# Kernel tuning notes

Measured on AMD Instinct MI355X. Metric: run time of the kernel, lower is better.

The kernel has to match this reference:

```python
import jax, jax.numpy as jnp
import numpy as np

N_NODES = 100000
N_EDGES = 1600000
D_IN, D_HID, D_OUT = 64, 64, 4


def _nnconv(x, src, dst, e, W_edge, b_edge, W_root, bias, n_nodes, d_in, d_out):
    """PyG NNConv with edge net Linear(1, d_in*d_out), aggr='add'.

    Theta_e = reshape(e * W_edge + b_edge, [d_in, d_out])  (linear in scalar e)
    => message_e = x[src] @ Theta_e = e * (x[src] @ Wm) + x[src] @ Bm
    out_i = sum_{e: dst=i} message_e + x_i @ W_root + bias
    """
    Wm = W_edge.reshape(d_in, d_out)   # edge-linear weight, factored
    Bm = b_edge.reshape(d_in, d_out)   # edge-linear bias, factored
    xj = x[src]                        # [E, d_in] irregular gather
    msg = e * (xj @ Wm) + xj @ Bm      # [E, d_out]; e is [E,1], broadcasts
    agg = jax.ops.segment_sum(msg, dst, num_segments=n_nodes)  # scatter-add
    return agg + x @ W_root + bias


def setup_inputs() -> dict:
    key = jax.random.key(0)
    ks = jax.random.split(key, 16)
    s = 0.05
    inp = {
        "x": jax.random.normal(ks[0], (N_NODES, D_IN), jnp.float32),
        "edge_index": jax.random.randint(ks[1], (2, N_EDGES), 0, N_NODES, jnp.int64 if jax.config.jax_enable_x64 else jnp.int32),
        "edge_attr": jax.random.uniform(ks[2], (N_EDGES, 1), jnp.float32),
        # layer 1: D_IN -> D_HID
        "We1": jax.random.normal(ks[3], (D_IN * D_HID,), jnp.float32) * s,
        "be1": jax.random.normal(ks[4], (D_IN * D_HID,), jnp.float32) * s,
        "Wr1": jax.random.normal(ks[5], (D_IN, D_HID), jnp.float32) * s,
        "b1": jnp.zeros((D_HID,), jnp.float32),
        # layer 2: D_HID -> D_HID
        "We2": jax.random.normal(ks[6], (D_HID * D_HID,), jnp.float32) * s,
        "be2": jax.random.normal(ks[7], (D_HID * D_HID,), jnp.float32) * s,
        "Wr2": jax.random.normal(ks[8], (D_HID, D_HID), jnp.float32) * s,
        "b2": jnp.zeros((D_HID,), jnp.float32),
        # layer 3: D_HID -> D_OUT
        "We3": jax.random.normal(ks[9], (D_HID * D_OUT,), jnp.float32) * s,
        "be3": jax.random.normal(ks[10], (D_HID * D_OUT,), jnp.float32) * s,
        "Wr3": jax.random.normal(ks[11], (D_HID, D_OUT), jnp.float32) * s,
        "b3": jnp.zeros((D_OUT,), jnp.float32),
    }
    return inp


def reference(x, edge_index, edge_attr,
              We1, be1, Wr1, b1,
              We2, be2, Wr2, b2,
              We3, be3, Wr3, b3):
    src, dst = edge_index[0], edge_index[1]  # source_to_target flow
    n = x.shape[0]
    h = _nnconv(x, src, dst, edge_attr, We1, be1, Wr1, b1, n, D_IN, D_HID)
    h = jax.nn.relu(h)  # dropout is a no-op at inference
    h = _nnconv(h, src, dst, edge_attr, We2, be2, Wr2, b2, n, D_HID, D_HID)
    h = jax.nn.relu(h)
    h = _nnconv(h, src, dst, edge_attr, We3, be3, Wr3, b3, n, D_HID, D_OUT)
    return jax.nn.log_softmax(h, axis=1)
```

## Files before the change

kernel.cpp:

```cpp
#include <hip/hip_runtime.h>
#include <math.h>

#define D 64
#define NBUCK 392
#define CAPB 4736
#define PART_BLOCKS 256

typedef __attribute__((ext_vector_type(4))) float f32x4;
typedef __attribute__((ext_vector_type(8))) _Float16 f16x8;
typedef __attribute__((ext_vector_type(2))) _Float16 f16x2;

__device__ __forceinline__ unsigned short f2h(float f) {
  return __builtin_bit_cast(unsigned short, (_Float16)f);
}
__device__ __forceinline__ f16x2 as_h2(unsigned u) { return __builtin_bit_cast(f16x2, u); }
__device__ __forceinline__ unsigned bcu(f16x2 v) { return __builtin_bit_cast(unsigned, v); }
__device__ __forceinline__ unsigned packH2(float a, float b) {
  f16x2 v; v.x = (_Float16)a; v.y = (_Float16)b;
  return __builtin_bit_cast(unsigned, v);
}


__global__ void wprep(const float* __restrict__ We1, const float* __restrict__ be1,
                      const float* __restrict__ Wr1, const float* __restrict__ We2,
                      const float* __restrict__ be2, const float* __restrict__ Wr2,
                      const float* __restrict__ We3, const float* __restrict__ be3,
                      const float* __restrict__ Wr3, unsigned short* __restrict__ Wt) {
  int l = blockIdx.x;
  if (l == 2) {
    unsigned short* Wt3 = Wt + 24576;
    for (int idx = threadIdx.x; idx < 1024; idx += 256) {
      int r = idx >> 6, k = idx & 63;
      int sel = r >> 2, o = r & 3;
      float v = (sel == 0) ? We3[k * 4 + o]
              : (sel == 1) ? be3[k * 4 + o]
              : (sel == 2) ? Wr3[k * 4 + o] : 0.f;
      Wt3[idx] = f2h(v);
    }
    return;
  }
  const float* We = l ? We2 : We1;
  const float* be = l ? be2 : be1;
  const float* Wr = l ? Wr2 : Wr1;
  for (int idx = threadIdx.x; idx < 12288; idx += 256) {
    int o = idx / 192, k = idx % 192;
    float v = (k < 64)  ? We[k * 64 + o]
            : (k < 128) ? be[(k - 64) * 64 + o]
                        : Wr[(k - 128) * 64 + o];
    Wt[l * 12288 + idx] = f2h(v);
  }
}

__global__ __launch_bounds__(256) void xprep(const float* __restrict__ x,
                                             unsigned short* __restrict__ xb, int n64) {
  int idx = (blockIdx.x * 256 + threadIdx.x) * 4;
  if (idx >= n64) return;
  float4 v = *(const float4*)(x + idx);
  ushort4 o;
  o.x = f2h(v.x); o.y = f2h(v.y); o.z = f2h(v.z); o.w = f2h(v.w);
  *(ushort4*)(xb + idx) = o;
}

__global__ __launch_bounds__(256) void transformC(
    const unsigned short* __restrict__ Sb, const unsigned short* __restrict__ hb,
    const unsigned short* __restrict__ WtP, const float* __restrict__ b,
    unsigned short* __restrict__ hbOut, int n) {
  __shared__ uint4 ldsW4[1536];
  char* ldsW = (char*)ldsW4;
  int t = threadIdx.x;
  const uint4* wg = (const uint4*)WtP;
#pragma unroll
  for (int i = 0; i < 6; ++i) {
    int idx = t + i * 256;
    int off = idx * 16;
    int row = idx / 24;
    *(uint4*)(ldsW + (off ^ ((row & 7) << 4))) = wg[idx];
  }
  __syncthreads();
  int wid = t >> 6, lane = t & 63;
  int n0 = blockIdx.x * 64 + wid * 16;
  if (n0 >= n) return;
  int arow = lane & 15, g = lane >> 4;
  int nodeA = min(n0 + arow, n - 1);
  const unsigned short* Sp = Sb + (size_t)nodeA * 128;
  f16x8 a[6];
#pragma unroll
  for (int c = 0; c < 4; ++c)
    a[c] = *(const f16x8*)(Sp + c * 32 + g * 8);
  const unsigned short* hp = hb + (size_t)nodeA * 64;
  a[4] = *(const f16x8*)(hp + g * 8);
  a[5] = *(const f16x8*)(hp + 32 + g * 8);

  f32x4 acc[4];
#pragma unroll
  for (int tt = 0; tt < 4; ++tt) acc[tt] = (f32x4){0.f, 0.f, 0.f, 0.f};
#pragma unroll
  for (int tt = 0; tt < 4; ++tt) {
    int o = tt * 16 + arow;
    int sw = (o & 7) << 4;
    int rb = o * 384;
#pragma unroll
    for (int c = 0; c < 6; ++c) {
      f16x8 bf = *(const f16x8*)(ldsW + ((rb + c * 64 + g * 16) ^ sw));
      acc[tt] = __builtin_amdgcn_mfma_f32_16x16x32_f16(a[c], bf, acc[tt], 0, 0, 0);
    }
  }
#pragma unroll
  for (int tt = 0; tt < 4; ++tt) {
    float bb = b[tt * 16 + arow];
#pragma unroll
    for (int r2 = 0; r2 < 4; ++r2) {
      int nd = n0 + g * 4 + r2;
      if (nd < n)
        hbOut[(size_t)nd * 64 + tt * 16 + arow] = f2h(fmaxf(acc[tt][r2] + bb, 0.f));
    }
  }
}

__global__ __launch_bounds__(256) void transform3M(
    const unsigned short* __restrict__ hb, const unsigned short* __restrict__ Wt3,
    const float* __restrict__ b, unsigned* __restrict__ yz3p,
    float* __restrict__ agg3, int n) {
  int t = threadIdx.x;
  int wid = t >> 6, lane = t & 63;
  int n0 = blockIdx.x * 64 + wid * 16;
  if (n0 >= n) return;
  int arow = lane & 15, g = lane >> 4;
  int nodeA = min(n0 + arow, n - 1);
  const unsigned short* hp = hb + (size_t)nodeA * 64;
  f16x8 a0 = *(const f16x8*)(hp + g * 8);
  f16x8 a1 = *(const f16x8*)(hp + 32 + g * 8);
  f16x8 b0 = *(const f16x8*)(Wt3 + arow * 64 + g * 8);
  f16x8 b1 = *(const f16x8*)(Wt3 + arow * 64 + 32 + g * 8);
  f32x4 acc = (f32x4){0.f, 0.f, 0.f, 0.f};
  acc = __builtin_amdgcn_mfma_f32_16x16x32_f16(a0, b0, acc, 0, 0, 0);
  acc = __builtin_amdgcn_mfma_f32_16x16x32_f16(a1, b1, acc, 0, 0, 0);
  float bb = (arow < 4) ? b[arow] : 0.f;
#pragma unroll
  for (int r2 = 0; r2 < 4; ++r2) {
    float zv = __shfl_xor(acc[r2], 4, 64);
    float rv = __shfl_xor(acc[r2], 8, 64);
    int nd = n0 + g * 4 + r2;
    if (arow < 4 && nd < n) {
      yz3p[(size_t)nd * 4 + arow] = packH2(acc[r2], zv);
      agg3[(size_t)nd * 4 + arow] = rv + bb;
    }
  }
}


__global__ __launch_bounds__(256) void histA(const int* __restrict__ ei,
                                             int* __restrict__ hist, int ne) {
  __shared__ int h[NBUCK];
  int t = threadIdx.x;
  for (int i = t; i < NBUCK; i += 256) h[i] = 0;
  __syncthreads();
  int chunk = (ne + PART_BLOCKS - 1) / PART_BLOCKS;
  int e0 = blockIdx.x * chunk;
  int e1 = min(ne, e0 + chunk);
  for (int e = e0 + t; e < e1; e += 256)
    atomicAdd(&h[ei[ne + e] >> 8], 1);
  __syncthreads();
  for (int i = t; i < NBUCK; i += 256) hist[blockIdx.x * NBUCK + i] = h[i];
}

__global__ __launch_bounds__(256) void scanCols(int* __restrict__ hist,
                                                int* __restrict__ gTotal) {
  __shared__ int wsum[4];
  int b = blockIdx.x;
  int t = threadIdx.x;
  int v = hist[t * NBUCK + b];
  int lane = t & 63, wid = t >> 6;
  int inc = v;
#pragma unroll
  for (int d = 1; d < 64; d <<= 1) {
    int u = __shfl_up(inc, d, 64);
    if (lane >= d) inc += u;
  }
  if (lane == 63) wsum[wid] = inc;
  __syncthreads();
  if (t == 0) {
    int a = 0;
#pragma unroll
    for (int w = 0; w < 4; ++w) { int tmp = wsum[w]; wsum[w] = a; a += tmp; }
  }
  __syncthreads();
  int excl = wsum[wid] + inc - v;
  hist[t * NBUCK + b] = b * CAPB + excl;
  if (t == 255) gTotal[b] = excl + v;
}

__global__ __launch_bounds__(256) void scatterC(
    const int* __restrict__ ei, const float* __restrict__ ea,
    const int* __restrict__ baseArr, uint2* __restrict__ edgesP, int ne) {
  __shared__ int cnt[NBUCK];
  __shared__ int lbase[NBUCK];
  int t = threadIdx.x;
  for (int i = t; i < NBUCK; i += 256) {
    cnt[i] = 0;
    lbase[i] = baseArr[blockIdx.x * NBUCK + i];
  }
  __syncthreads();
  int chunk = (ne + PART_BLOCKS - 1) / PART_BLOCKS;
  int e0 = blockIdx.x * chunk;
  int e1 = min(ne, e0 + chunk);
  for (int e = e0 + t; e < e1; e += 256) {
    unsigned s = (unsigned)ei[e];
    int dd = ei[ne + e];
    float ev = ea[e];
    unsigned abits = packH2(ev, ev);
    int bk = dd >> 8;
    int pos = atomicAdd(&cnt[bk], 1);
    edgesP[lbase[bk] + pos] = make_uint2(s | ((unsigned)(dd & 255) << 20), abits);
  }
}

__global__ __launch_bounds__(256) void placeK(
    const uint2* __restrict__ edgesP, const int* __restrict__ gTotal,
    uint2* __restrict__ edgeS, int* __restrict__ offS, int* __restrict__ offE,
    int n) {
  __shared__ int deg[256];
  __shared__ int cur[256];
  __shared__ int wsum[4];
  int b = blockIdx.x;
  int t = threadIdx.x;
  int base = b * CAPB;
  int cnt = gTotal[b];
  int n0 = b << 8;
  int nn = min(256, n - n0);
  deg[t] = 0;
  __syncthreads();
  for (int i = t; i < cnt; i += 256)
    atomicAdd(&deg[edgesP[base + i].x >> 20], 1);
  __syncthreads();
  int v = deg[t];
  int lane = t & 63, wid = t >> 6;
  int inc = v;
#pragma unroll
  for (int d2 = 1; d2 < 64; d2 <<= 1) {
    int u = __shfl_up(inc, d2, 64);
    if (lane >= d2) inc += u;
  }
  if (lane == 63) wsum[wid] = inc;
  __syncthreads();
  if (t == 0) {
    int a = 0;
#pragma unroll
    for (int w = 0; w < 4; ++w) { int tmp = wsum[w]; wsum[w] = a; a += tmp; }
  }
  __syncthreads();
  int excl = wsum[wid] + inc - v;
  cur[t] = excl;
  if (t < nn) {
    offS[n0 + t] = base + excl;
    offE[n0 + t] = base + excl + v;
  }
  __syncthreads();
  for (int i = t; i < cnt; i += 256) {
    uint2 ent = edgesP[base + i];
    int dl = ent.x >> 20;
    int slot = base + atomicAdd(&cur[dl], 1);
    edgeS[slot] = make_uint2(ent.x & 0xFFFFFu, ent.y);
  }
}

__global__ __launch_bounds__(256) void gather2(
    const int* __restrict__ offS, const int* __restrict__ offE,
    const uint2* __restrict__ edgeS, const unsigned short* __restrict__ hb,
    unsigned short* __restrict__ Sb, int n) {
  int node = (blockIdx.x * 256 + threadIdx.x) >> 6;
  int lane = threadIdx.x & 63;
  if (node >= n) return;
  int grp = lane >> 3, l8 = lane & 7;
  int j0 = offS[node];
  int jend = offE[node];
  f16x2 s1[4], s0[4];
#pragma unroll
  for (int q = 0; q < 4; ++q) { s1[q] = (f16x2)0; s0[q] = (f16x2)0; }
  int j = j0 + grp;
#pragma unroll 1
  for (; j + 8 < jend; j += 16) {
    uint2 edA = edgeS[j];
    uint2 edB = edgeS[j + 8];
    uint4 rA = *(const uint4*)(hb + (size_t)edA.x * 64 + l8 * 8);
    uint4 rB = *(const uint4*)(hb + (size_t)edB.x * 64 + l8 * 8);
    f16x2 eA = as_h2(edA.y);
    f16x2 eB = as_h2(edB.y);
    f16x2 hA[4] = {as_h2(rA.x), as_h2(rA.y), as_h2(rA.z), as_h2(rA.w)};
    f16x2 hB[4] = {as_h2(rB.x), as_h2(rB.y), as_h2(rB.z), as_h2(rB.w)};
#pragma unroll
    for (int q = 0; q < 4; ++q) {
      s1[q] += hA[q] * eA; s0[q] += hA[q];
      s1[q] += hB[q] * eB; s0[q] += hB[q];
    }
  }
  if (j < jend) {
    uint2 ed = edgeS[j];
    uint4 r = *(const uint4*)(hb + (size_t)ed.x * 64 + l8 * 8);
    f16x2 e = as_h2(ed.y);
    f16x2 h[4] = {as_h2(r.x), as_h2(r.y), as_h2(r.z), as_h2(r.w)};
#pragma unroll
    for (int q = 0; q < 4; ++q) { s1[q] += h[q] * e; s0[q] += h[q]; }
  }
#pragma unroll
  for (int q = 0; q < 4; ++q) {
    s1[q] += as_h2(__shfl_xor(bcu(s1[q]), 8, 64));
    s1[q] += as_h2(__shfl_xor(bcu(s1[q]), 16, 64));
    s1[q] += as_h2(__shfl_xor(bcu(s1[q]), 32, 64));
    s0[q] += as_h2(__shfl_xor(bcu(s0[q]), 8, 64));
    s0[q] += as_h2(__shfl_xor(bcu(s0[q]), 16, 64));
    s0[q] += as_h2(__shfl_xor(bcu(s0[q]), 32, 64));
  }
  if (grp == 0) {
    unsigned short* sp = Sb + (size_t)node * 128 + l8 * 8;
    *(uint4*)sp = make_uint4(bcu(s1[0]), bcu(s1[1]), bcu(s1[2]), bcu(s1[3]));
    *(uint4*)(sp + 64) = make_uint4(bcu(s0[0]), bcu(s0[1]), bcu(s0[2]), bcu(s0[3]));
  }
}

__global__ __launch_bounds__(256) void gather4_logsm(
    const int* __restrict__ offS, const int* __restrict__ offE,
    const uint2* __restrict__ edgeS, const unsigned* __restrict__ yz3p,
    const float* __restrict__ agg3, float* __restrict__ out, int n) {
  int idx = blockIdx.x * 256 + threadIdx.x;
  int node = idx >> 2;
  int o = idx & 3;
  if (node >= n) return;
  int j = offS[node];
  int jend = offE[node];
  float acc = agg3[(size_t)node * 4 + o];
#pragma unroll 1
  for (; j < jend; ++j) {
    uint2 ed = edgeS[j];
    f16x2 yz = as_h2(yz3p[(size_t)ed.x * 4 + o]);
    float e = (float)as_h2(ed.y).x;
    acc += fmaf(e, (float)yz.x, (float)yz.y);
  }
  float m = acc;
  m = fmaxf(m, __shfl_xor(m, 1, 4));
  m = fmaxf(m, __shfl_xor(m, 2, 4));
  float s = expf(acc - m);
  s += __shfl_xor(s, 1, 4);
  s += __shfl_xor(s, 2, 4);
  out[(size_t)node * 4 + o] = acc - m - logf(s);
}


extern "C" void kernel_launch(void* const* d_in, const int* in_sizes, int n_in,
                              void* d_out, int out_size, void* d_ws, size_t ws_size,
                              hipStream_t stream) {
  const float* x = (const float*)d_in[0];
  const int* ei = (const int*)d_in[1];
  const float* ea = (const float*)d_in[2];
  const float* We1 = (const float*)d_in[3];
  const float* be1 = (const float*)d_in[4];
  const float* Wr1 = (const float*)d_in[5];
  const float* b1 = (const float*)d_in[6];
  const float* We2 = (const float*)d_in[7];
  const float* be2 = (const float*)d_in[8];
  const float* Wr2 = (const float*)d_in[9];
  const float* b2 = (const float*)d_in[10];
  const float* We3 = (const float*)d_in[11];
  const float* be3 = (const float*)d_in[12];
  const float* Wr3 = (const float*)d_in[13];
  const float* b3 = (const float*)d_in[14];

  const int N = in_sizes[0] / D;
  const int E = in_sizes[2];
  const size_t EREG = (size_t)NBUCK * CAPB;

  char* ws = (char*)d_ws;
  uint2* edgeS = (uint2*)ws;
  unsigned short* Sb = (unsigned short*)(ws + EREG * 8);
  unsigned short* xb = Sb + (size_t)N * 128;
  unsigned short* hb2 = xb + (size_t)N * 64;
  unsigned* yz3p = (unsigned*)(hb2 + (size_t)N * 64);
  float* agg3 = (float*)(yz3p + (size_t)N * 4);
  int* offS = (int*)(agg3 + (size_t)N * 4);
  int* offE = offS + N;
  int* gTotal = offE + N;
  int* hist = gTotal + NBUCK;
  unsigned short* Wt = (unsigned short*)(hist + PART_BLOCKS * NBUCK);
  uint2* edgesP = (uint2*)Sb;
  unsigned short* hb3 = xb;
  float* out = (float*)d_out;

  int tblocksM = (N + 63) / 64;
  int g64blocks = (int)(((long long)N * 64 + 255) / 256);
  int g4blocks = (int)(((long long)N * 4 + 255) / 256);
  int xblocks = (int)(((long long)N * 64 / 4 + 255) / 256);

  wprep<<<3, 256, 0, stream>>>(We1, be1, Wr1, We2, be2, Wr2, We3, be3, Wr3, Wt);
  xprep<<<xblocks, 256, 0, stream>>>(x, xb, N * 64);
  histA<<<PART_BLOCKS, 256, 0, stream>>>(ei, hist, E);
  scanCols<<<NBUCK, 256, 0, stream>>>(hist, gTotal);
  scatterC<<<PART_BLOCKS, 256, 0, stream>>>(ei, ea, hist, edgesP, E);
  placeK<<<NBUCK, 256, 0, stream>>>(edgesP, gTotal, edgeS, offS, offE, N);

  gather2<<<g64blocks, 256, 0, stream>>>(offS, offE, edgeS, xb, Sb, N);
  transformC<<<tblocksM, 256, 0, stream>>>(Sb, xb, Wt, b1, hb2, N);
  gather2<<<g64blocks, 256, 0, stream>>>(offS, offE, edgeS, hb2, Sb, N);
  transformC<<<tblocksM, 256, 0, stream>>>(Sb, hb2, Wt + 12288, b2, hb3, N);
  transform3M<<<tblocksM, 256, 0, stream>>>(hb3, Wt + 24576, b3, yz3p, agg3, N);
  gather4_logsm<<<g4blocks, 256, 0, stream>>>(offS, offE, edgeS, yz3p, agg3, out, N);
}
```

Measured before the change: 296.4 us.

## Fuse prep kernels, fuse layer-3 transform into layer-2 epilogue, unroll final gather

```diff
diff --git a/kernel.cpp b/kernel.cpp
--- a/kernel.cpp
+++ b/kernel.cpp
@@ -20,52 +20,72 @@
   return __builtin_bit_cast(unsigned, v);
 }
 
-
-__global__ void wprep(const float* __restrict__ We1, const float* __restrict__ be1,
-                      const float* __restrict__ Wr1, const float* __restrict__ We2,
-                      const float* __restrict__ be2, const float* __restrict__ Wr2,
-                      const float* __restrict__ We3, const float* __restrict__ be3,
-                      const float* __restrict__ Wr3, unsigned short* __restrict__ Wt) {
-  int l = blockIdx.x;
-  if (l == 2) {
-    unsigned short* Wt3 = Wt + 24576;
-    for (int idx = threadIdx.x; idx < 1024; idx += 256) {
-      int r = idx >> 6, k = idx & 63;
-      int sel = r >> 2, o = r & 3;
-      float v = (sel == 0) ? We3[k * 4 + o]
-              : (sel == 1) ? be3[k * 4 + o]
-              : (sel == 2) ? Wr3[k * 4 + o] : 0.f;
-      Wt3[idx] = f2h(v);
-    }
-    return;
-  }
-  const float* We = l ? We2 : We1;
-  const float* be = l ? be2 : be1;
-  const float* Wr = l ? Wr2 : Wr1;
-  for (int idx = threadIdx.x; idx < 12288; idx += 256) {
-    int o = idx / 192, k = idx % 192;
-    float v = (k < 64)  ? We[k * 64 + o]
-            : (k < 128) ? be[(k - 64) * 64 + o]
-                        : Wr[(k - 128) * 64 + o];
-    Wt[l * 12288 + idx] = f2h(v);
-  }
-}
-
-__global__ __launch_bounds__(256) void xprep(const float* __restrict__ x,
-                                             unsigned short* __restrict__ xb, int n64) {
-  int idx = (blockIdx.x * 256 + threadIdx.x) * 4;
-  if (idx >= n64) return;
-  float4 v = *(const float4*)(x + idx);
-  ushort4 o;
-  o.x = f2h(v.x); o.y = f2h(v.y); o.z = f2h(v.z); o.w = f2h(v.w);
-  *(ushort4*)(xb + idx) = o;
-}
-
+__global__ __launch_bounds__(256) void prepK(
+    const int* __restrict__ ei, int ne,
+    const float* __restrict__ x, unsigned short* __restrict__ xb, int n64,
+    const float* __restrict__ We1, const float* __restrict__ be1,
+    const float* __restrict__ Wr1, const float* __restrict__ We2,
+    const float* __restrict__ be2, const float* __restrict__ Wr2,
+    const float* __restrict__ We3, const float* __restrict__ be3,
+    const float* __restrict__ Wr3, unsigned short* __restrict__ Wt,
+    int* __restrict__ hist) {
+  __shared__ int h[NBUCK];
+  int bid = blockIdx.x;
+  int t = threadIdx.x;
+  if (bid < PART_BLOCKS) {
+    for (int i = t; i < NBUCK; i += 256) h[i] = 0;
+    __syncthreads();
+    int chunk = (ne + PART_BLOCKS - 1) / PART_BLOCKS;
+    int e0 = bid * chunk;
+    int e1 = min(ne, e0 + chunk);
+    for (int e = e0 + t; e < e1; e += 256)
+      atomicAdd(&h[ei[ne + e] >> 8], 1);
+    __syncthreads();
+    for (int i = t; i < NBUCK; i += 256) hist[bid * NBUCK + i] = h[i];
+  } else if (bid < PART_BLOCKS + 3) {
+    int l = bid - PART_BLOCKS;
+    if (l == 2) {
+      unsigned short* Wt3 = Wt + 24576;
+      for (int idx = t; idx < 1024; idx += 256) {
+        int r = idx >> 6, k = idx & 63;
+        int sel = r >> 2, o = r & 3;
+        float v = (sel == 0) ? We3[k * 4 + o]
+                : (sel == 1) ? be3[k * 4 + o]
+                : (sel == 2) ? Wr3[k * 4 + o] : 0.f;
+        Wt3[idx] = f2h(v);
+      }
+    } else {
+      const float* We = l ? We2 : We1;
+      const float* be = l ? be2 : be1;
+      const float* Wr = l ? Wr2 : Wr1;
+      for (int idx = t; idx < 12288; idx += 256) {
+        int o = idx / 192, k = idx % 192;
+        float v = (k < 64)  ? We[k * 64 + o]
+                : (k < 128) ? be[(k - 64) * 64 + o]
+                            : Wr[(k - 128) * 64 + o];
+        Wt[l * 12288 + idx] = f2h(v);
+      }
+    }
+  } else {
+    int idx = ((bid - PART_BLOCKS - 3) * 256 + t) * 4;
+    if (idx < n64) {
+      float4 v = *(const float4*)(x + idx);
+      ushort4 o;
+      o.x = f2h(v.x); o.y = f2h(v.y); o.z = f2h(v.z); o.w = f2h(v.w);
+      *(ushort4*)(xb + idx) = o;
+    }
+  }
+}
+
+template <bool RELU, bool LAST>
 __global__ __launch_bounds__(256) void transformC(
     const unsigned short* __restrict__ Sb, const unsigned short* __restrict__ hb,
     const unsigned short* __restrict__ WtP, const float* __restrict__ b,
-    unsigned short* __restrict__ hbOut, int n) {
+    unsigned short* __restrict__ hbOut,
+    const unsigned short* __restrict__ Wt3, const float* __restrict__ b3,
+    unsigned* __restrict__ yz3p, float* __restrict__ agg3, int n) {
   __shared__ uint4 ldsW4[1536];
+  __shared__ unsigned short ldsH[4][1024];
   char* ldsW = (char*)ldsW4;
   int t = threadIdx.x;
   const uint4* wg = (const uint4*)WtP;
@@ -105,64 +125,52 @@
       acc[tt] = __builtin_amdgcn_mfma_f32_16x16x32_f16(a[c], bf, acc[tt], 0, 0, 0);
     }
   }
-#pragma unroll
-  for (int tt = 0; tt < 4; ++tt) {
-    float bb = b[tt * 16 + arow];
+  if (!LAST) {
+#pragma unroll
+    for (int tt = 0; tt < 4; ++tt) {
+      float bb = b[tt * 16 + arow];
+#pragma unroll
+      for (int r2 = 0; r2 < 4; ++r2) {
+        int nd = n0 + g * 4 + r2;
+        if (nd < n)
+          hbOut[(size_t)nd * 64 + tt * 16 + arow] = f2h(fmaxf(acc[tt][r2] + bb, 0.f));
+      }
+    }
+  } else {
+    char* ldsC = (char*)ldsH[wid];
+#pragma unroll
+    for (int tt = 0; tt < 4; ++tt) {
+      float bb = b[tt * 16 + arow];
+#pragma unroll
+      for (int r2 = 0; r2 < 4; ++r2) {
+        int ndl = g * 4 + r2;
+        int boff = ndl * 128 + (tt * 16 + arow) * 2;
+        *(unsigned short*)(ldsC + (boff ^ ((ndl & 7) << 4))) =
+            f2h(fmaxf(acc[tt][r2] + bb, 0.f));
+      }
+    }
+    int sw2 = (arow & 7) << 4;
+    f16x8 a3a = *(const f16x8*)(ldsC + ((arow * 128 + g * 16) ^ sw2));
+    f16x8 a3b = *(const f16x8*)(ldsC + ((arow * 128 + 64 + g * 16) ^ sw2));
+    f16x8 b3a = *(const f16x8*)(Wt3 + arow * 64 + g * 8);
+    f16x8 b3b = *(const f16x8*)(Wt3 + arow * 64 + 32 + g * 8);
+    f32x4 acc3 = (f32x4){0.f, 0.f, 0.f, 0.f};
+    acc3 = __builtin_amdgcn_mfma_f32_16x16x32_f16(a3a, b3a, acc3, 0, 0, 0);
+    acc3 = __builtin_amdgcn_mfma_f32_16x16x32_f16(a3b, b3b, acc3, 0, 0, 0);
+    float bb3 = (arow < 4) ? b3[arow] : 0.f;
 #pragma unroll
     for (int r2 = 0; r2 < 4; ++r2) {
+      float zv = __shfl_xor(acc3[r2], 4, 64);
+      float rv = __shfl_xor(acc3[r2], 8, 64);
       int nd = n0 + g * 4 + r2;
-      if (nd < n)
-        hbOut[(size_t)nd * 64 + tt * 16 + arow] = f2h(fmaxf(acc[tt][r2] + bb, 0.f));
-    }
-  }
-}
-
-__global__ __launch_bounds__(256) void transform3M(
-    const unsigned short* __restrict__ hb, const unsigned short* __restrict__ Wt3,
-    const float* __restrict__ b, unsigned* __restrict__ yz3p,
-    float* __restrict__ agg3, int n) {
-  int t = threadIdx.x;
-  int wid = t >> 6, lane = t & 63;
-  int n0 = blockIdx.x * 64 + wid * 16;
-  if (n0 >= n) return;
-  int arow = lane & 15, g = lane >> 4;
-  int nodeA = min(n0 + arow, n - 1);
-  const unsigned short* hp = hb + (size_t)nodeA * 64;
-  f16x8 a0 = *(const f16x8*)(hp + g * 8);
-  f16x8 a1 = *(const f16x8*)(hp + 32 + g * 8);
-  f16x8 b0 = *(const f16x8*)(Wt3 + arow * 64 + g * 8);
-  f16x8 b1 = *(const f16x8*)(Wt3 + arow * 64 + 32 + g * 8);
-  f32x4 acc = (f32x4){0.f, 0.f, 0.f, 0.f};
-  acc = __builtin_amdgcn_mfma_f32_16x16x32_f16(a0, b0, acc, 0, 0, 0);
-  acc = __builtin_amdgcn_mfma_f32_16x16x32_f16(a1, b1, acc, 0, 0, 0);
-  float bb = (arow < 4) ? b[arow] : 0.f;
-#pragma unroll
-  for (int r2 = 0; r2 < 4; ++r2) {
-    float zv = __shfl_xor(acc[r2], 4, 64);
-    float rv = __shfl_xor(acc[r2], 8, 64);
-    int nd = n0 + g * 4 + r2;
-    if (arow < 4 && nd < n) {
-      yz3p[(size_t)nd * 4 + arow] = packH2(acc[r2], zv);
-      agg3[(size_t)nd * 4 + arow] = rv + bb;
-    }
-  }
-}
-
-
-__global__ __launch_bounds__(256) void histA(const int* __restrict__ ei,
-                                             int* __restrict__ hist, int ne) {
-  __shared__ int h[NBUCK];
-  int t = threadIdx.x;
-  for (int i = t; i < NBUCK; i += 256) h[i] = 0;
-  __syncthreads();
-  int chunk = (ne + PART_BLOCKS - 1) / PART_BLOCKS;
-  int e0 = blockIdx.x * chunk;
-  int e1 = min(ne, e0 + chunk);
-  for (int e = e0 + t; e < e1; e += 256)
-    atomicAdd(&h[ei[ne + e] >> 8], 1);
-  __syncthreads();
-  for (int i = t; i < NBUCK; i += 256) hist[blockIdx.x * NBUCK + i] = h[i];
-}
+      if (arow < 4 && nd < n) {
+        yz3p[(size_t)nd * 4 + arow] = packH2(acc3[r2], zv);
+        agg3[(size_t)nd * 4 + arow] = rv + bb3;
+      }
+    }
+  }
+}
+
 
 __global__ __launch_bounds__(256) void scanCols(int* __restrict__ hist,
                                                 int* __restrict__ gTotal) {
@@ -330,11 +338,18 @@
   int jend = offE[node];
   float acc = agg3[(size_t)node * 4 + o];
 #pragma unroll 1
-  for (; j < jend; ++j) {
+  for (; j + 1 < jend; j += 2) {
+    uint2 e0 = edgeS[j];
+    uint2 e1 = edgeS[j + 1];
+    f16x2 yz0 = as_h2(yz3p[(size_t)e0.x * 4 + o]);
+    f16x2 yz1 = as_h2(yz3p[(size_t)e1.x * 4 + o]);
+    acc += fmaf((float)as_h2(e0.y).x, (float)yz0.x, (float)yz0.y);
+    acc += fmaf((float)as_h2(e1.y).x, (float)yz1.x, (float)yz1.y);
+  }
+  if (j < jend) {
     uint2 ed = edgeS[j];
     f16x2 yz = as_h2(yz3p[(size_t)ed.x * 4 + o]);
-    float e = (float)as_h2(ed.y).x;
-    acc += fmaf(e, (float)yz.x, (float)yz.y);
+    acc += fmaf((float)as_h2(ed.y).x, (float)yz.x, (float)yz.y);
   }
   float m = acc;
   m = fmaxf(m, __shfl_xor(m, 1, 4));
@@ -382,7 +397,6 @@
   int* hist = gTotal + NBUCK;
   unsigned short* Wt = (unsigned short*)(hist + PART_BLOCKS * NBUCK);
   uint2* edgesP = (uint2*)Sb;
-  unsigned short* hb3 = xb;
   float* out = (float*)d_out;
 
   int tblocksM = (N + 63) / 64;
@@ -390,17 +404,17 @@
   int g4blocks = (int)(((long long)N * 4 + 255) / 256);
   int xblocks = (int)(((long long)N * 64 / 4 + 255) / 256);
 
-  wprep<<<3, 256, 0, stream>>>(We1, be1, Wr1, We2, be2, Wr2, We3, be3, Wr3, Wt);
-  xprep<<<xblocks, 256, 0, stream>>>(x, xb, N * 64);
-  histA<<<PART_BLOCKS, 256, 0, stream>>>(ei, hist, E);
+  prepK<<<PART_BLOCKS + 3 + xblocks, 256, 0, stream>>>(
+      ei, E, x, xb, N * 64, We1, be1, Wr1, We2, be2, Wr2, We3, be3, Wr3, Wt, hist);
   scanCols<<<NBUCK, 256, 0, stream>>>(hist, gTotal);
   scatterC<<<PART_BLOCKS, 256, 0, stream>>>(ei, ea, hist, edgesP, E);
   placeK<<<NBUCK, 256, 0, stream>>>(edgesP, gTotal, edgeS, offS, offE, N);
 
   gather2<<<g64blocks, 256, 0, stream>>>(offS, offE, edgeS, xb, Sb, N);
-  transformC<<<tblocksM, 256, 0, stream>>>(Sb, xb, Wt, b1, hb2, N);
+  transformC<false, false><<<tblocksM, 256, 0, stream>>>(
+      Sb, xb, Wt, b1, hb2, nullptr, nullptr, nullptr, nullptr, N);
   gather2<<<g64blocks, 256, 0, stream>>>(offS, offE, edgeS, hb2, Sb, N);
-  transformC<<<tblocksM, 256, 0, stream>>>(Sb, hb2, Wt + 12288, b2, hb3, N);
-  transform3M<<<tblocksM, 256, 0, stream>>>(hb3, Wt + 24576, b3, yz3p, agg3, N);
+  transformC<true, true><<<tblocksM, 256, 0, stream>>>(
+      Sb, hb2, Wt + 12288, b2, nullptr, Wt + 24576, b3, yz3p, agg3, N);
   gather4_logsm<<<g4blocks, 256, 0, stream>>>(offS, offE, edgeS, yz3p, agg3, out, N);
 }
```

Result: faster. 267.9 us (-9.6%).
